# Kernel tuning notes

Measured on AMD Instinct MI355X. Metric: run time of the kernel, lower is better.

The kernel has to match this reference:

```python
import jax, jax.numpy as jnp
import numpy as np

B, LQ, LKV = 32, 512, 512
SIZE, H = 512, 8
HD = SIZE // H
SCALE = 1.0 / np.sqrt(HD)
LN_EPS = 1e-5


def layer_norm(x, w, b):
    mu = jnp.mean(x, axis=-1, keepdims=True)
    var = jnp.mean(jnp.square(x - mu), axis=-1, keepdims=True)
    return (x - mu) * jax.lax.rsqrt(var + LN_EPS) * w + b


def setup_inputs() -> dict:
    key = jax.random.key(0)
    ks = jax.random.split(key, 8)
    s = 0.02
    return {
        "query": jax.random.normal(ks[0], (B, LQ, SIZE), jnp.float32),
        "key_value": jax.random.normal(ks[1], (B, LKV, SIZE), jnp.float32),
        "Wq": jax.random.normal(ks[2], (SIZE, SIZE), jnp.float32) * s,
        "bq": jnp.zeros((SIZE,), jnp.float32),
        "Wk": jax.random.normal(ks[3], (SIZE, SIZE), jnp.float32) * s,
        "bk": jnp.zeros((SIZE,), jnp.float32),
        "Wv": jax.random.normal(ks[4], (SIZE, SIZE), jnp.float32) * s,
        "bv": jnp.zeros((SIZE,), jnp.float32),
        "Wo": jax.random.normal(ks[5], (SIZE, SIZE), jnp.float32) * s,
        "bo": jnp.zeros((SIZE,), jnp.float32),
        "ln0_w": jnp.ones((SIZE,), jnp.float32),
        "ln0_b": jnp.zeros((SIZE,), jnp.float32),
        "ln1_w": jnp.ones((SIZE,), jnp.float32),
        "ln1_b": jnp.zeros((SIZE,), jnp.float32),
    }


def reference(query, key_value, Wq, bq, Wk, bk, Wv, bv, Wo, bo, ln0_w, ln0_b, ln1_w, ln1_b):
    b, lq, _ = query.shape
    lkv = key_value.shape[1]
    # projections
    q = query @ Wq.T + bq          # [B, Lq, SIZE]
    k = key_value @ Wk.T + bk      # [B, Lkv, SIZE]
    v = key_value @ Wv.T + bv
    # split heads: torch cat(split(head_size, 2), 0) == [B,L,H,HD] view with head axis separate
    qh = q.reshape(b, lq, H, HD)
    kh = k.reshape(b, lkv, H, HD)
    vh = v.reshape(b, lkv, H, HD)
    # attention scores [B, H, Lq, Lkv]
    A_ = jnp.einsum("bqhd,bkhd->bhqk", qh, kh) * SCALE
    # signed softmax: tanh(A_) * softmax(sqrt(A_^2 + 0.01)) over keys
    A = jnp.tanh(A_) * jax.nn.softmax(jnp.sqrt(jnp.square(A_) + 0.01), axis=-1)
    # residual q + attention output, merge heads back
    oh = qh + jnp.einsum("bhqk,bkhd->bqhd", A, vh)   # [B, Lq, H, HD]
    output = oh.reshape(b, lq, SIZE)
    output = layer_norm(output, ln0_w, ln0_b)
    output = output + jax.nn.relu(output @ Wo.T + bo)
    output = layer_norm(output, ln1_w, ln1_b)
    return output
```

## Files before the change

kernel.cpp:

```cpp
#include <hip/hip_runtime.h>

#define SIZE_D 512
#define HEADS  8
#define HDIM   64
#define BATCH  32
#define SEQ    512
#define SCALE_F 0.125f
#define NROWS  (BATCH * SEQ)

typedef __attribute__((ext_vector_type(8))) short bf16x8;
typedef __attribute__((ext_vector_type(4))) float f32x4;
typedef __attribute__((ext_vector_type(4))) unsigned int u32x4;

__device__ __forceinline__ unsigned short f2bf(float f) {
    union { float f; unsigned int u; } c{f};
    unsigned int x = c.u;
    x += 0x7fffu + ((x >> 16) & 1u);
    return (unsigned short)(x >> 16);
}
__device__ __forceinline__ float bf2f(unsigned short u) {
    union { unsigned int i; float f; } c;
    c.i = (unsigned int)u << 16;
    return c.f;
}
__device__ __forceinline__ void gload_lds16(const unsigned short* g, unsigned short* l) {
    __builtin_amdgcn_global_load_lds(
        (const __attribute__((address_space(1))) unsigned int*)g,
        (__attribute__((address_space(3))) unsigned int*)l, 16, 0, 0);
}

__global__ __launch_bounds__(256) void cvt_act(const float* __restrict__ q,
                                               const float* __restrict__ kv,
                                               unsigned short* __restrict__ dq,
                                               unsigned short* __restrict__ dkv) {
    const float* s = blockIdx.y ? kv : q;
    unsigned short* d = blockIdx.y ? dkv : dq;
    const int n = NROWS * SIZE_D;
    const int stride = gridDim.x * blockDim.x * 4;
    for (int i = (blockIdx.x * blockDim.x + threadIdx.x) * 4; i < n; i += stride) {
        const float4 v = *reinterpret_cast<const float4*>(s + i);
        ushort4 o;
        o.x = f2bf(v.x); o.y = f2bf(v.y); o.z = f2bf(v.z); o.w = f2bf(v.w);
        *reinterpret_cast<ushort4*>(d + i) = o;
    }
}

__global__ __launch_bounds__(256) void cvt_w4(const float* __restrict__ w0,
                                              const float* __restrict__ w1,
                                              const float* __restrict__ w2,
                                              const float* __restrict__ w3,
                                              unsigned short* __restrict__ d) {
    const float* srcs[4] = {w0, w1, w2, w3};
    const float* s = srcs[blockIdx.y];
    unsigned short* dst = d + (size_t)blockIdx.y * (SIZE_D * SIZE_D);
    const int n = SIZE_D * SIZE_D;
    const int stride = gridDim.x * blockDim.x * 4;
    for (int i = (blockIdx.x * blockDim.x + threadIdx.x) * 4; i < n; i += stride) {
        const float4 v = *reinterpret_cast<const float4*>(s + i);
        ushort4 o;
        o.x = f2bf(v.x); o.y = f2bf(v.y); o.z = f2bf(v.z); o.w = f2bf(v.w);
        *reinterpret_cast<ushort4*>(dst + i) = o;
    }
}

__global__ __launch_bounds__(256, 2) void gemm_proj3(const unsigned short* __restrict__ Qbf,
                                                     const unsigned short* __restrict__ KVbf,
                                                     const unsigned short* __restrict__ Wall,
                                                     const float* __restrict__ bq,
                                                     const float* __restrict__ bk,
                                                     const float* __restrict__ bv,
                                                     unsigned short* __restrict__ Qh,
                                                     unsigned short* __restrict__ Kh,
                                                     unsigned short* __restrict__ Vt) {
    __shared__ __align__(16) unsigned short Ad[2][128 * 64];
    __shared__ __align__(16) unsigned short Bd[2][128 * 64];

    const int tid  = threadIdx.x;
    const int wv   = tid >> 6;
    const int lane = tid & 63;
    const int y    = blockIdx.y;
    const int bm   = blockIdx.x * 128;
    const int bn   = y * 128;
    const int wr   = wv >> 1;
    const int wc   = wv & 1;

    const unsigned short* A = (y < 4) ? Qbf : KVbf;

    auto stage = [&](int buf, int t) {
        const int k0 = t * 64;
#pragma unroll
        for (int i = 0; i < 4; ++i) {
            const int o     = (wv * 32 + i * 8) * 128 + lane * 16;
            const int row   = o >> 7;
            const int inrow = (o & 127) ^ ((row & 7) << 4);
            const int col   = inrow >> 1;
            gload_lds16(A + (size_t)(bm + row) * SIZE_D + k0 + col, &Ad[buf][o >> 1]);
            gload_lds16(Wall + (size_t)(bn + row) * SIZE_D + k0 + col, &Bd[buf][o >> 1]);
        }
    };

    f32x4 acc[4][4];
#pragma unroll
    for (int mt = 0; mt < 4; ++mt)
#pragma unroll
        for (int nt = 0; nt < 4; ++nt) acc[mt][nt] = (f32x4){0.f, 0.f, 0.f, 0.f};

    stage(0, 0);
    __syncthreads();
    int cur = 0;

    for (int t = 0; t < 8; ++t) {
        if (t < 7) stage(cur ^ 1, t + 1);

        bf16x8 af[2][4], bfr[2][4];
#pragma unroll
        for (int kc = 0; kc < 2; ++kc) {
#pragma unroll
            for (int mt = 0; mt < 4; ++mt) {
                const int r = wr * 64 + mt * 16 + (lane & 15);
                int byte = r * 128 + kc * 64 + (lane >> 4) * 16;
                byte ^= (r & 7) << 4;
                af[kc][mt] = *reinterpret_cast<const bf16x8*>(
                    reinterpret_cast<const char*>(&Ad[cur][0]) + byte);
            }
#pragma unroll
            for (int nt = 0; nt < 4; ++nt) {
                const int r = wc * 64 + nt * 16 + (lane & 15);
                int byte = r * 128 + kc * 64 + (lane >> 4) * 16;
                byte ^= (r & 7) << 4;
                bfr[kc][nt] = *reinterpret_cast<const bf16x8*>(
                    reinterpret_cast<const char*>(&Bd[cur][0]) + byte);
            }
        }
#pragma unroll
        for (int kc = 0; kc < 2; ++kc)
#pragma unroll
            for (int mt = 0; mt < 4; ++mt)
#pragma unroll
                for (int nt = 0; nt < 4; ++nt)
                    acc[mt][nt] = __builtin_amdgcn_mfma_f32_16x16x32_bf16(
                        af[kc][mt], bfr[kc][nt], acc[mt][nt], 0, 0, 0);

        __syncthreads();
        cur ^= 1;
    }

    if (y < 8) {
        const float* bias = (y < 4) ? bq : bk;
        unsigned short* D = (y < 4) ? Qh : Kh;
        const int coff = (y < 4) ? 0 : 512;
#pragma unroll
        for (int nt = 0; nt < 4; ++nt) {
            const int colL = bn - coff + wc * 64 + nt * 16 + (lane & 15);
            const float bc = bias[colL];
            const int h = colL >> 6, dd = colL & 63;
#pragma unroll
            for (int mt = 0; mt < 4; ++mt) {
                const int row0 = bm + wr * 64 + mt * 16 + (lane >> 4) * 4;
#pragma unroll
                for (int r = 0; r < 4; ++r) {
                    const int row = row0 + r;
                    const int b_ = row >> 9, l = row & 511;
                    float z = acc[mt][nt][r] + bc;
                    if (y >= 4) z *= SCALE_F;
                    D[(((size_t)b_ * HEADS + h) * SEQ + l) * HDIM + dd] = f2bf(z);
                }
            }
        }
    } else {
#pragma unroll
        for (int nt = 0; nt < 4; ++nt) {
            const int c2 = bn - 1024 + wc * 64 + nt * 16 + (lane & 15);
            const float bc = bv[c2];
            const int hV = c2 >> 6, dV = c2 & 63;
#pragma unroll
            for (int mt = 0; mt < 4; ++mt) {
                const int row0 = bm + wr * 64 + mt * 16 + (lane >> 4) * 4;
                const int b_ = row0 >> 9, kv = row0 & 511;
                ushort4 pk;
                pk.x = f2bf(acc[mt][nt][0] + bc);
                pk.y = f2bf(acc[mt][nt][1] + bc);
                pk.z = f2bf(acc[mt][nt][2] + bc);
                pk.w = f2bf(acc[mt][nt][3] + bc);
                *reinterpret_cast<ushort4*>(
                    &Vt[(((size_t)b_ * HEADS + hV) * HDIM + dV) * SEQ + kv]) = pk;
            }
        }
    }
}

__global__ __launch_bounds__(256, 2) void attn_mfma(const unsigned short* __restrict__ Qh,
                                                    const unsigned short* __restrict__ Kh,
                                                    const unsigned short* __restrict__ Vt,
                                                    float* __restrict__ outq) {
    __shared__ __align__(16) unsigned short Kt[2][64 * 64];
    __shared__ __align__(16) unsigned short Vs[2][64 * 64];

    const int tid  = threadIdx.x;
    const int wv   = tid >> 6;
    const int lane = tid & 63;
    const int bh   = blockIdx.x;
    const int b    = bh >> 3;
    const int h    = bh & 7;
    const int g    = lane >> 4;

    const unsigned short* Qb = Qh + (size_t)bh * (SEQ * HDIM);
    const unsigned short* Kb = Kh + (size_t)bh * (SEQ * HDIM);
    const unsigned short* Vb = Vt + (size_t)bh * (HDIM * SEQ);

    const int m0 = blockIdx.y * 256 + wv * 64;

    auto stageKV = [&](int buf, int t) {
        const int kv0 = t * 64;
#pragma unroll
        for (int i = 0; i < 2; ++i) {
            const int o   = i * 4096 + tid * 16;
            const int row = o >> 7;
            const int in  = (o & 127) ^ ((row & 7) << 4);
            gload_lds16(Kb + (size_t)(kv0 + row) * HDIM + (in >> 1), &Kt[buf][o >> 1]);
            gload_lds16(Vb + (size_t)row * SEQ + kv0 + (in >> 1), &Vs[buf][o >> 1]);
        }
    };

    bf16x8 qf[4][2];
#pragma unroll
    for (int mt = 0; mt < 4; ++mt)
#pragma unroll
        for (int kc = 0; kc < 2; ++kc) {
            const int m = m0 + mt * 16 + (lane & 15);
            union { u32x4 u; bf16x8 v; } cv;
            cv.u = *reinterpret_cast<const u32x4*>(
                Qb + (size_t)m * HDIM + kc * 32 + g * 8);
            qf[mt][kc] = cv.v;
        }

    f32x4 oacc[4][4];
    float esum[4] = {0.f, 0.f, 0.f, 0.f};
#pragma unroll
    for (int mt = 0; mt < 4; ++mt)
#pragma unroll
        for (int x = 0; x < 4; ++x) oacc[mt][x] = (f32x4){0.f, 0.f, 0.f, 0.f};

    stageKV(0, 0);
    __syncthreads();
    int cur = 0;

    for (int t = 0; t < 8; ++t) {
        if (t < 7) stageKV(cur ^ 1, t + 1);

        f32x4 sacc[4][4];
#pragma unroll
        for (int nt = 0; nt < 4; ++nt)
#pragma unroll
            for (int mt = 0; mt < 4; ++mt) sacc[nt][mt] = (f32x4){0.f, 0.f, 0.f, 0.f};

#pragma unroll
        for (int kc = 0; kc < 2; ++kc) {
            bf16x8 kf[4];
#pragma unroll
            for (int nt = 0; nt < 4; ++nt) {
                const int kvl = nt * 16 + (lane & 15);
                int byte = kvl * 128 + kc * 64 + g * 16;
                byte ^= (kvl & 7) << 4;
                kf[nt] = *reinterpret_cast<const bf16x8*>(
                    reinterpret_cast<const char*>(&Kt[cur][0]) + byte);
            }
#pragma unroll
            for (int nt = 0; nt < 4; ++nt)
#pragma unroll
                for (int mt = 0; mt < 4; ++mt)
                    sacc[nt][mt] = __builtin_amdgcn_mfma_f32_16x16x32_bf16(
                        kf[nt], qf[mt][kc], sacc[nt][mt], 0, 0, 0);
        }

        bf16x8 pa[2][4];
#pragma unroll
        for (int c = 0; c < 2; ++c)
#pragma unroll
            for (int mt = 0; mt < 4; ++mt) {
                float w[8];
#pragma unroll
                for (int j = 0; j < 8; ++j) {
                    const float s  = sacc[2 * c + (j >> 2)][mt][j & 3];
                    const float a  = fminf(fabsf(s), 30.0f);
                    const float tt = __expf(a);
                    const float t2 = tt * tt;
                    const float u  = __builtin_amdgcn_sqrtf(fmaf(s, s, 0.01f));
                    const float dl = u - a;
                    const float ed = fmaf(dl, fmaf(dl, fmaf(dl, 0.16666667f, 0.5f), 1.0f), 1.0f);
                    const float eu = tt * ed;
                    esum[mt] += eu;
                    const float th = (t2 - 1.0f) * __builtin_amdgcn_rcpf(t2 + 1.0f);
                    w[j] = __builtin_copysignf(th * eu, s);
                }
                union { unsigned int u[4]; bf16x8 v; } pk;
#pragma unroll
                for (int p = 0; p < 4; ++p)
                    pk.u[p] = (__float_as_uint(w[2 * p + 1]) & 0xffff0000u) |
                              (__float_as_uint(w[2 * p]) >> 16);
                pa[c][mt] = pk.v;
            }

#pragma unroll
        for (int c = 0; c < 2; ++c) {
            bf16x8 vf[4];
#pragma unroll
            for (int dt = 0; dt < 4; ++dt) {
                const int d = dt * 16 + (lane & 15);
                const int swz = (d & 7) << 4;
                const int rowb = d * 128;
                uint2 lo = *reinterpret_cast<const uint2*>(
                    reinterpret_cast<const char*>(&Vs[cur][0]) +
                    (rowb + (((c * 32 + 4 * g) * 2) ^ swz)));
                uint2 hi = *reinterpret_cast<const uint2*>(
                    reinterpret_cast<const char*>(&Vs[cur][0]) +
                    (rowb + (((c * 32 + 16 + 4 * g) * 2) ^ swz)));
                union { unsigned int u[4]; bf16x8 v; } cvb;
                cvb.u[0] = lo.x; cvb.u[1] = lo.y;
                cvb.u[2] = hi.x; cvb.u[3] = hi.y;
                vf[dt] = cvb.v;
            }
#pragma unroll
            for (int mt = 0; mt < 4; ++mt)
#pragma unroll
                for (int dt = 0; dt < 4; ++dt)
                    oacc[mt][dt] = __builtin_amdgcn_mfma_f32_16x16x32_bf16(
                        pa[c][mt], vf[dt], oacc[mt][dt], 0, 0, 0);
        }

        __syncthreads();
        cur ^= 1;
    }

    float rden[4];
#pragma unroll
    for (int mt = 0; mt < 4; ++mt) {
        float e = esum[mt];
        e += __shfl_xor(e, 16);
        e += __shfl_xor(e, 32);
        rden[mt] = __builtin_amdgcn_rcpf(e);
    }
    float rr_[4][4];
#pragma unroll
    for (int mt = 0; mt < 4; ++mt)
#pragma unroll
        for (int r = 0; r < 4; ++r)
            rr_[mt][r] = __shfl(rden[mt], g * 4 + r);

#pragma unroll
    for (int mt = 0; mt < 4; ++mt)
#pragma unroll
        for (int dt = 0; dt < 4; ++dt)
#pragma unroll
            for (int r = 0; r < 4; ++r) {
                const int m = m0 + mt * 16 + g * 4 + r;
                const int d = dt * 16 + (lane & 15);
                const float qv = bf2f(Qb[(size_t)m * HDIM + d]);
                outq[((size_t)b * SEQ + m) * SIZE_D + h * HDIM + d] =
                    qv + oacc[mt][dt][r] * rr_[mt][r];
            }
}

__global__ __launch_bounds__(256) void ln0_bf16(const float* __restrict__ in,
                                                const float* __restrict__ w,
                                                const float* __restrict__ b,
                                                unsigned short* __restrict__ outb) {
    const int row = blockIdx.x;
    const int tid = threadIdx.x;
    const float2 x = *reinterpret_cast<const float2*>(&in[(size_t)row * SIZE_D + tid * 2]);

    float s  = x.x + x.y;
    float sq = x.x * x.x + x.y * x.y;
#pragma unroll
    for (int off = 32; off > 0; off >>= 1) {
        s  += __shfl_xor(s, off);
        sq += __shfl_xor(sq, off);
    }
    __shared__ float rs[4], rq[4];
    const int wv = tid >> 6;
    if ((tid & 63) == 0) { rs[wv] = s; rq[wv] = sq; }
    __syncthreads();
    s  = rs[0] + rs[1] + rs[2] + rs[3];
    sq = rq[0] + rq[1] + rq[2] + rq[3];

    const float mu  = s * (1.0f / SIZE_D);
    const float var = sq * (1.0f / SIZE_D) - mu * mu;
    const float rr  = rsqrtf(var + 1e-5f);

    const float2 wv2 = *reinterpret_cast<const float2*>(&w[tid * 2]);
    const float2 bv2 = *reinterpret_cast<const float2*>(&b[tid * 2]);
    ushort2 ob;
    ob.x = f2bf((x.x - mu) * rr * wv2.x + bv2.x);
    ob.y = f2bf((x.y - mu) * rr * wv2.y + bv2.y);
    *reinterpret_cast<ushort2*>(&outb[(size_t)row * SIZE_D + tid * 2]) = ob;
}

__global__ __launch_bounds__(512, 2) void oproj_ln(const unsigned short* __restrict__ X,
                                                   const unsigned short* __restrict__ W,
                                                   const float* __restrict__ bo,
                                                   const float* __restrict__ g1,
                                                   const float* __restrict__ b1,
                                                   float* __restrict__ out) {
    __shared__ __align__(16) unsigned short Ad[2][64 * 32];
    __shared__ __align__(16) unsigned short Bd[2][512 * 32];
    __shared__ float red[64][8][2];
    __shared__ float stat[64][2];

    const int tid  = threadIdx.x;
    const int wv   = tid >> 6;
    const int lane = tid & 63;
    const int bm   = blockIdx.x * 64;

    auto stage = [&](int buf, int t) {
        const int k0 = t * 32;
        if (tid < 256) {
            const int o   = tid * 16;
            const int row = o >> 6;
            const int in  = (o & 63) ^ (((row >> 1) & 3) << 4);
            gload_lds16(X + (size_t)(bm + row) * SIZE_D + k0 + (in >> 1), &Ad[buf][o >> 1]);
        }
#pragma unroll
        for (int i = 0; i < 4; ++i) {
            const int o   = i * 8192 + tid * 16;
            const int row = o >> 6;
            const int in  = (o & 63) ^ (((row >> 1) & 3) << 4);
            gload_lds16(W + (size_t)row * SIZE_D + k0 + (in >> 1), &Bd[buf][o >> 1]);
        }
    };

    f32x4 acc[4][4];
#pragma unroll
    for (int mt = 0; mt < 4; ++mt)
#pragma unroll
        for (int nt = 0; nt < 4; ++nt) acc[mt][nt] = (f32x4){0.f, 0.f, 0.f, 0.f};

    stage(0, 0);
    __syncthreads();
    int cur = 0;

    for (int t = 0; t < 16; ++t) {
        if (t < 15) stage(cur ^ 1, t + 1);

        bf16x8 af[4], bfr[4];
#pragma unroll
        for (int mt = 0; mt < 4; ++mt) {
            const int r = mt * 16 + (lane & 15);
            int byte = r * 64 + (lane >> 4) * 16;
            byte ^= ((r >> 1) & 3) << 4;
            af[mt] = *reinterpret_cast<const bf16x8*>(
                reinterpret_cast<const char*>(&Ad[cur][0]) + byte);
        }
#pragma unroll
        for (int nt = 0; nt < 4; ++nt) {
            const int r = wv * 64 + nt * 16 + (lane & 15);
            int byte = r * 64 + (lane >> 4) * 16;
            byte ^= ((r >> 1) & 3) << 4;
            bfr[nt] = *reinterpret_cast<const bf16x8*>(
                reinterpret_cast<const char*>(&Bd[cur][0]) + byte);
        }
#pragma unroll
        for (int mt = 0; mt < 4; ++mt)
#pragma unroll
            for (int nt = 0; nt < 4; ++nt)
                acc[mt][nt] = __builtin_amdgcn_mfma_f32_16x16x32_bf16(
                    af[mt], bfr[nt], acc[mt][nt], 0, 0, 0);

        __syncthreads();
        cur ^= 1;
    }

#pragma unroll
    for (int nt = 0; nt < 4; ++nt) {
        const int n  = wv * 64 + nt * 16 + (lane & 15);
        const float bc = bo[n];
#pragma unroll
        for (int mt = 0; mt < 4; ++mt) {
            const int row0 = bm + mt * 16 + (lane >> 4) * 4;
#pragma unroll
            for (int r = 0; r < 4; ++r) {
                const float R = bf2f(X[(size_t)(row0 + r) * SIZE_D + n]);
                acc[mt][nt][r] = R + fmaxf(acc[mt][nt][r] + bc, 0.0f);
            }
        }
    }

    float ps[4][4], pq[4][4];
#pragma unroll
    for (int mt = 0; mt < 4; ++mt)
#pragma unroll
        for (int r = 0; r < 4; ++r) {
            float s = 0.f, q = 0.f;
#pragma unroll
            for (int nt = 0; nt < 4; ++nt) {
                const float v = acc[mt][nt][r];
                s += v; q += v * v;
            }
#pragma unroll
            for (int off = 1; off <= 8; off <<= 1) {
                s += __shfl_xor(s, off);
                q += __shfl_xor(q, off);
            }
            ps[mt][r] = s; pq[mt][r] = q;
        }
    {
        const int mtw = (lane & 15) >> 2, rw = lane & 3;
        const int rowL = mtw * 16 + (lane >> 4) * 4 + rw;
        red[rowL][wv][0] = ps[mtw][rw];
        red[rowL][wv][1] = pq[mtw][rw];
    }
    __syncthreads();
    if (tid < 64) {
        float s = 0.f, q = 0.f;
#pragma unroll
        for (int w8 = 0; w8 < 8; ++w8) { s += red[tid][w8][0]; q += red[tid][w8][1]; }
        const float mu  = s * (1.0f / SIZE_D);
        const float var = q * (1.0f / SIZE_D) - mu * mu;
        stat[tid][0] = mu;
        stat[tid][1] = rsqrtf(var + 1e-5f);
    }
    __syncthreads();

#pragma unroll
    for (int nt = 0; nt < 4; ++nt) {
        const int n = wv * 64 + nt * 16 + (lane & 15);
        const float g = g1[n], bb = b1[n];
#pragma unroll
        for (int mt = 0; mt < 4; ++mt) {
#pragma unroll
            for (int r = 0; r < 4; ++r) {
                const int rowL = mt * 16 + (lane >> 4) * 4 + r;
                const float y = (acc[mt][nt][r] - stat[rowL][0]) * stat[rowL][1];
                out[(size_t)(bm + rowL) * SIZE_D + n] = y * g + bb;
            }
        }
    }
}

extern "C" void kernel_launch(void* const* d_in, const int* in_sizes, int n_in,
                              void* d_out, int out_size, void* d_ws, size_t ws_size,
                              hipStream_t stream) {
    const float* query = (const float*)d_in[0];
    const float* keyv  = (const float*)d_in[1];
    const float* Wq    = (const float*)d_in[2];
    const float* bq    = (const float*)d_in[3];
    const float* Wk    = (const float*)d_in[4];
    const float* bk    = (const float*)d_in[5];
    const float* Wv    = (const float*)d_in[6];
    const float* bv    = (const float*)d_in[7];
    const float* Wo    = (const float*)d_in[8];
    const float* bo    = (const float*)d_in[9];
    const float* ln0w  = (const float*)d_in[10];
    const float* ln0b  = (const float*)d_in[11];
    const float* ln1w  = (const float*)d_in[12];
    const float* ln1b  = (const float*)d_in[13];
    float* out = (float*)d_out;

    char* ws = (char*)d_ws;
    unsigned short* Qbf  = (unsigned short*)ws;
    unsigned short* KVbf = (unsigned short*)(ws + ((size_t)16 << 20));
    float*          qbuf = (float*)ws;
    unsigned short* Qh   = (unsigned short*)(ws + ((size_t)32 << 20));
    unsigned short* Xbf  = Qh;
    unsigned short* Kh   = (unsigned short*)(ws + ((size_t)48 << 20));
    unsigned short* Vt   = (unsigned short*)(ws + ((size_t)64 << 20));
    unsigned short* Wbf  = (unsigned short*)(ws + ((size_t)80 << 20));
    unsigned short* WoB  = Wbf + 786432;

    cvt_act<<<dim3(1024, 2), 256, 0, stream>>>(query, keyv, Qbf, KVbf);
    cvt_w4<<<dim3(64, 4), 256, 0, stream>>>(Wq, Wk, Wv, Wo, Wbf);

    gemm_proj3<<<dim3(128, 12), 256, 0, stream>>>(Qbf, KVbf, Wbf, bq, bk, bv, Qh, Kh, Vt);

    attn_mfma<<<dim3(BATCH * HEADS, 2), 256, 0, stream>>>(Qh, Kh, Vt, qbuf);

    ln0_bf16<<<NROWS, 256, 0, stream>>>(qbuf, ln0w, ln0b, Xbf);

    oproj_ln<<<NROWS / 64, 512, 0, stream>>>(Xbf, WoB, bo, ln1w, ln1b, out);
}
```

Baseline: 166.4 us.

## Fuse fp32-to-bf16 activation conversion into projection GEMM A-tile staging

Removes the separate cvt_act kernel and has gemm_proj3 read fp32 query/key_value directly. The fp32 values are held in registers, converted to bf16 and written to LDS after the MFMA loop, replacing the async global-to-LDS load. This saves a full read and write pass over the activations and one kernel launch. In exchange, each A tile is read as fp32 (twice the bytes) by each of the 4 column blocks, and register pressure rises. The rounding also changes from round-to-nearest-even to round-half-up.

```diff
diff --git a/kernel.cpp b/kernel.cpp
--- a/kernel.cpp
+++ b/kernel.cpp
@@ -23,26 +23,14 @@
     c.i = (unsigned int)u << 16;
     return c.f;
 }
+__device__ __forceinline__ unsigned int pack2bf(float lo, float hi) {
+    return ((__float_as_uint(hi) + 0x8000u) & 0xffff0000u) |
+           ((__float_as_uint(lo) + 0x8000u) >> 16);
+}
 __device__ __forceinline__ void gload_lds16(const unsigned short* g, unsigned short* l) {
     __builtin_amdgcn_global_load_lds(
         (const __attribute__((address_space(1))) unsigned int*)g,
         (__attribute__((address_space(3))) unsigned int*)l, 16, 0, 0);
-}
-
-__global__ __launch_bounds__(256) void cvt_act(const float* __restrict__ q,
-                                               const float* __restrict__ kv,
-                                               unsigned short* __restrict__ dq,
-                                               unsigned short* __restrict__ dkv) {
-    const float* s = blockIdx.y ? kv : q;
-    unsigned short* d = blockIdx.y ? dkv : dq;
-    const int n = NROWS * SIZE_D;
-    const int stride = gridDim.x * blockDim.x * 4;
-    for (int i = (blockIdx.x * blockDim.x + threadIdx.x) * 4; i < n; i += stride) {
-        const float4 v = *reinterpret_cast<const float4*>(s + i);
-        ushort4 o;
-        o.x = f2bf(v.x); o.y = f2bf(v.y); o.z = f2bf(v.z); o.w = f2bf(v.w);
-        *reinterpret_cast<ushort4*>(d + i) = o;
-    }
 }
 
 __global__ __launch_bounds__(256) void cvt_w4(const float* __restrict__ w0,
@@ -63,8 +51,8 @@
     }
 }
 
-__global__ __launch_bounds__(256, 2) void gemm_proj3(const unsigned short* __restrict__ Qbf,
-                                                     const unsigned short* __restrict__ KVbf,
+__global__ __launch_bounds__(256, 2) void gemm_proj3(const float* __restrict__ query,
+                                                     const float* __restrict__ keyv,
                                                      const unsigned short* __restrict__ Wall,
                                                      const float* __restrict__ bq,
                                                      const float* __restrict__ bk,
@@ -84,17 +72,41 @@
     const int wr   = wv >> 1;
     const int wc   = wv & 1;
 
-    const unsigned short* A = (y < 4) ? Qbf : KVbf;
-
-    auto stage = [&](int buf, int t) {
+    const float* A = (y < 4) ? query : keyv;
+
+    float4 areg[4][2];
+
+    auto loadA = [&](int t) {
         const int k0 = t * 64;
 #pragma unroll
         for (int i = 0; i < 4; ++i) {
-            const int o     = (wv * 32 + i * 8) * 128 + lane * 16;
-            const int row   = o >> 7;
-            const int inrow = (o & 127) ^ ((row & 7) << 4);
-            const int col   = inrow >> 1;
-            gload_lds16(A + (size_t)(bm + row) * SIZE_D + k0 + col, &Ad[buf][o >> 1]);
+            const int o   = (wv * 32 + i * 8) * 128 + lane * 16;
+            const int row = o >> 7;
+            const int col = ((o & 127) ^ ((row & 7) << 4)) >> 1;
+            const float* src = A + (size_t)(bm + row) * SIZE_D + k0 + col;
+            areg[i][0] = *reinterpret_cast<const float4*>(src);
+            areg[i][1] = *reinterpret_cast<const float4*>(src + 4);
+        }
+    };
+    auto writeA = [&](int buf) {
+#pragma unroll
+        for (int i = 0; i < 4; ++i) {
+            const int o = (wv * 32 + i * 8) * 128 + lane * 16;
+            union { unsigned int u[4]; bf16x8 v; } pk;
+            pk.u[0] = pack2bf(areg[i][0].x, areg[i][0].y);
+            pk.u[1] = pack2bf(areg[i][0].z, areg[i][0].w);
+            pk.u[2] = pack2bf(areg[i][1].x, areg[i][1].y);
+            pk.u[3] = pack2bf(areg[i][1].z, areg[i][1].w);
+            *reinterpret_cast<bf16x8*>(&Ad[buf][o >> 1]) = pk.v;
+        }
+    };
+    auto stageW = [&](int buf, int t) {
+        const int k0 = t * 64;
+#pragma unroll
+        for (int i = 0; i < 4; ++i) {
+            const int o   = (wv * 32 + i * 8) * 128 + lane * 16;
+            const int row = o >> 7;
+            const int col = ((o & 127) ^ ((row & 7) << 4)) >> 1;
             gload_lds16(Wall + (size_t)(bn + row) * SIZE_D + k0 + col, &Bd[buf][o >> 1]);
         }
     };
@@ -105,12 +117,17 @@
 #pragma unroll
         for (int nt = 0; nt < 4; ++nt) acc[mt][nt] = (f32x4){0.f, 0.f, 0.f, 0.f};
 
-    stage(0, 0);
+    loadA(0);
+    stageW(0, 0);
+    writeA(0);
     __syncthreads();
     int cur = 0;
 
     for (int t = 0; t < 8; ++t) {
-        if (t < 7) stage(cur ^ 1, t + 1);
+        if (t < 7) {
+            loadA(t + 1);
+            stageW(cur ^ 1, t + 1);
+        }
 
         bf16x8 af[2][4], bfr[2][4];
 #pragma unroll
@@ -141,6 +158,7 @@
                     acc[mt][nt] = __builtin_amdgcn_mfma_f32_16x16x32_bf16(
                         af[kc][mt], bfr[kc][nt], acc[mt][nt], 0, 0, 0);
 
+        if (t < 7) writeA(cur ^ 1);
         __syncthreads();
         cur ^= 1;
     }
@@ -556,8 +574,6 @@
     float* out = (float*)d_out;
 
     char* ws = (char*)d_ws;
-    unsigned short* Qbf  = (unsigned short*)ws;
-    unsigned short* KVbf = (unsigned short*)(ws + ((size_t)16 << 20));
     float*          qbuf = (float*)ws;
     unsigned short* Qh   = (unsigned short*)(ws + ((size_t)32 << 20));
     unsigned short* Xbf  = Qh;
@@ -566,10 +582,9 @@
     unsigned short* Wbf  = (unsigned short*)(ws + ((size_t)80 << 20));
     unsigned short* WoB  = Wbf + 786432;
 
-    cvt_act<<<dim3(1024, 2), 256, 0, stream>>>(query, keyv, Qbf, KVbf);
     cvt_w4<<<dim3(64, 4), 256, 0, stream>>>(Wq, Wk, Wv, Wo, Wbf);
 
-    gemm_proj3<<<dim3(128, 12), 256, 0, stream>>>(Qbf, KVbf, Wbf, bq, bk, bv, Qh, Kh, Vt);
+    gemm_proj3<<<dim3(128, 12), 256, 0, stream>>>(query, keyv, Wbf, bq, bk, bv, Qh, Kh, Vt);
 
     attn_mfma<<<dim3(BATCH * HEADS, 2), 256, 0, stream>>>(Qh, Kh, Vt, qbuf);
 
```

New measurement: 163.8 us. Within noise of the previous version (-1.6%).
